# Kernel tuning notes

Hardware: AMD Instinct MI355X
Metric: run time of the kernel (lower is better)

The kernel has to match this reference:

```python
import jax, jax.numpy as jnp
import numpy as np

CHANNEL_ROT = 16
NUM_PIECES = 11
NUM_SQUARES = 64
NUM_FEATURES = NUM_PIECES * NUM_SQUARES * NUM_SQUARES  # 45056
NUM_VECTORS = NUM_SQUARES * NUM_SQUARES               # 4096
VECTOR_DIM = 256
BATCH = 1
TAU = 1.0


def setup_inputs() -> dict:
    key = jax.random.key(0)
    k1, k2, k3 = jax.random.split(key, 3)
    # learned parameter (torch.rand init)
    indices_logits = jax.random.uniform(k1, (NUM_FEATURES, NUM_VECTORS), dtype=jnp.float32)
    # shared vector codebook base (rolled per piece inside reference)
    shared_vectors_base = jax.random.normal(k2, (NUM_VECTORS, VECTOR_DIM), dtype=jnp.float32)
    # explicit gumbel noise so the gumbel-softmax sample is deterministic
    u = jax.random.uniform(k3, (BATCH, NUM_FEATURES, NUM_VECTORS), dtype=jnp.float32,
                           minval=1e-20, maxval=1.0)
    gumbel_noise = -jnp.log(-jnp.log(u))
    # forward arg; only its batch dim is used by the module
    active_features = jnp.zeros((BATCH, NUM_FEATURES), dtype=jnp.int32)
    return {"active_features": active_features,
            "indices_logits": indices_logits,
            "shared_vectors_base": shared_vectors_base,
            "gumbel_noise": gumbel_noise}


def reference(active_features, indices_logits, shared_vectors_base, gumbel_noise):
    B = gumbel_noise.shape[0]
    # per-piece shared vectors: channel-rolled copies of the base codebook (P, V, D)
    sv = jnp.stack([jnp.roll(shared_vectors_base, p * CHANNEL_ROT, axis=1)
                    for p in range(NUM_PIECES)])
    # soft gumbel-softmax sample over the NUM_VECTORS category dim: (B, F, V)
    probs = jax.nn.softmax((indices_logits[None, :, :] + gumbel_noise) / TAU, axis=-1)
    # per-piece einsum 'bqv,vd->bd' == sum probs over q first, then contract v
    q = NUM_FEATURES // NUM_PIECES  # 4096 features per piece
    piece_mass = probs.reshape(B, NUM_PIECES, q, NUM_VECTORS).sum(axis=2)  # (B, P, V)
    position_embedding = jnp.einsum('bpv,pvd->bd', piece_mass, sv)  # (B, D)
    return position_embedding
```

## Files before the change

kernel.cpp:

```cpp
#include <hip/hip_runtime.h>

#define V_DIM   4096
#define D_DIM   256
#define P_CNT   11
#define NB      128
#define ROWS_PB 32
#define P2_BLK  128
#define P2_ROWS 32

__global__ __launch_bounds__(256) void phase1_softmax_mass(
    const float* __restrict__ logits,
    const float* __restrict__ gumbel,
    float* __restrict__ mass)
{
    const int t    = threadIdx.x;
    const int lane = t & 63;
    const int wid  = t >> 6;
    const int b    = blockIdx.x;
    const int p    = b >> 7;
    const int sub  = b & (NB - 1);
    const size_t row0 = (size_t)p * V_DIM + (size_t)sub * ROWS_PB;

    __shared__ float red[8];

    float acc[16];
#pragma unroll
    for (int k = 0; k < 16; ++k) acc[k] = 0.f;

    const float4* lg = (const float4*)(logits + row0 * (size_t)V_DIM);
    const float4* gn = (const float4*)(gumbel + row0 * (size_t)V_DIM);

    float4 a[4], g[4];
#pragma unroll
    for (int k = 0; k < 4; ++k) {
        a[k] = lg[t + 256 * k];
        g[k] = gn[t + 256 * k];
    }

    for (int r = 0; r < ROWS_PB; ++r) {
        float4 a2[4], g2[4];
        const bool more = (r + 1 < ROWS_PB);
        if (more) {
            const float4* lg2 = lg + (size_t)(r + 1) * 1024;
            const float4* gn2 = gn + (size_t)(r + 1) * 1024;
#pragma unroll
            for (int k = 0; k < 4; ++k) {
                a2[k] = lg2[t + 256 * k];
                g2[k] = gn2[t + 256 * k];
            }
        }

        float e[16];
        float s = 0.f;
#pragma unroll
        for (int k = 0; k < 4; ++k) {
            e[4 * k + 0] = __expf(a[k].x + g[k].x);
            e[4 * k + 1] = __expf(a[k].y + g[k].y);
            e[4 * k + 2] = __expf(a[k].z + g[k].z);
            e[4 * k + 3] = __expf(a[k].w + g[k].w);
            s += (e[4 * k + 0] + e[4 * k + 1]) + (e[4 * k + 2] + e[4 * k + 3]);
        }

#pragma unroll
        for (int off = 32; off >= 1; off >>= 1)
            s += __shfl_xor(s, off, 64);
        const int slot = (r & 1) << 2;
        if (lane == 0) red[slot + wid] = s;
        __syncthreads();
        s = (red[slot + 0] + red[slot + 1]) + (red[slot + 2] + red[slot + 3]);
        const float inv = 1.f / s;

#pragma unroll
        for (int k = 0; k < 16; ++k) acc[k] += e[k] * inv;

        if (more) {
#pragma unroll
            for (int k = 0; k < 4; ++k) { a[k] = a2[k]; g[k] = g2[k]; }
        }
    }

    float* mp = mass + (size_t)p * V_DIM;
#pragma unroll
    for (int k = 0; k < 4; ++k) {
        const int j = 4 * (t + 256 * k);
        atomicAdd(mp + j + 0, acc[4 * k + 0]);
        atomicAdd(mp + j + 1, acc[4 * k + 1]);
        atomicAdd(mp + j + 2, acc[4 * k + 2]);
        atomicAdd(mp + j + 3, acc[4 * k + 3]);
    }
}

__global__ __launch_bounds__(256) void phase2_contract(
    const float* __restrict__ mass,
    const float* __restrict__ base,
    float* __restrict__ partial)
{
    __shared__ float sv[P2_ROWS][D_DIM];
    __shared__ float mt[P_CNT][P2_ROWS];

    const int t  = threadIdx.x;
    const int b  = blockIdx.x;
    const int v0 = b * P2_ROWS;

    const float4* bp  = (const float4*)(base + (size_t)v0 * D_DIM);
    float4*       svp = (float4*)&sv[0][0];
#pragma unroll
    for (int k = 0; k < 8; ++k) svp[t + 256 * k] = bp[t + 256 * k];

    for (int i = t; i < P_CNT * P2_ROWS; i += 256) {
        const int p  = i / P2_ROWS;
        const int vv = i - p * P2_ROWS;
        mt[p][vv] = mass[(size_t)p * V_DIM + v0 + vv];
    }
    __syncthreads();

    float a = 0.f;
    for (int v = 0; v < P2_ROWS; ++v) {
#pragma unroll
        for (int p = 0; p < P_CNT; ++p)
            a += mt[p][v] * sv[v][(t - 16 * p) & 255];
    }
    partial[(size_t)b * D_DIM + t] = a;
}

__global__ __launch_bounds__(256) void phase3_reduce(
    const float* __restrict__ partial,
    float* __restrict__ out)
{
    const int t = threadIdx.x;
    float s = 0.f;
#pragma unroll 8
    for (int b = 0; b < P2_BLK; ++b) s += partial[(size_t)b * D_DIM + t];
    out[t] = s;
}

extern "C" void kernel_launch(void* const* d_in, const int* in_sizes, int n_in,
                              void* d_out, int out_size, void* d_ws, size_t ws_size,
                              hipStream_t stream)
{
    const float* logits = (const float*)d_in[1];
    const float* base   = (const float*)d_in[2];
    const float* gumbel = (const float*)d_in[3];
    float* out = (float*)d_out;

    float* mass    = (float*)d_ws;
    float* partial = mass + (size_t)P_CNT * V_DIM;

    hipMemsetAsync(d_ws, 0, (size_t)P_CNT * V_DIM * sizeof(float), stream);

    phase1_softmax_mass<<<dim3(P_CNT * NB), 256, 0, stream>>>(logits, gumbel, mass);
    phase2_contract<<<dim3(P2_BLK), 256, 0, stream>>>(mass, base, partial);
    phase3_reduce<<<dim3(1), 256, 0, stream>>>(partial, out);
}
```

Measured before the change: 287.4 us.

## Replace atomic mass accumulation with per-block partials and a separate reduction kernel

Phase 1 blocks now write their 4096-wide partial mass vectors to a workspace buffer with float4 stores instead of issuing scalar float atomics into a shared per-piece array. A new reduction kernel sums the 128 partials per piece, which also removes the memset. The per-row __syncthreads is swapped for a raw s_waitcnt plus s_barrier. The cost is about 23 MB of extra workspace writes and reads plus one more kernel launch, traded against atomic contention.

```diff
diff --git a/kernel.cpp b/kernel.cpp
--- a/kernel.cpp
+++ b/kernel.cpp
@@ -5,21 +5,20 @@
 #define P_CNT   11
 #define NB      128
 #define ROWS_PB 32
+#define NBLK    (P_CNT * NB)
 #define P2_BLK  128
 #define P2_ROWS 32
 
-__global__ __launch_bounds__(256) void phase1_softmax_mass(
+__global__ __launch_bounds__(256) void phase1_softmax_part(
     const float* __restrict__ logits,
     const float* __restrict__ gumbel,
-    float* __restrict__ mass)
+    float* __restrict__ part)
 {
     const int t    = threadIdx.x;
     const int lane = t & 63;
     const int wid  = t >> 6;
     const int b    = blockIdx.x;
-    const int p    = b >> 7;
-    const int sub  = b & (NB - 1);
-    const size_t row0 = (size_t)p * V_DIM + (size_t)sub * ROWS_PB;
+    const size_t row0 = (size_t)b * ROWS_PB;
 
     __shared__ float red[8];
 
@@ -66,9 +65,12 @@
             s += __shfl_xor(s, off, 64);
         const int slot = (r & 1) << 2;
         if (lane == 0) red[slot + wid] = s;
-        __syncthreads();
+        asm volatile("s_waitcnt lgkmcnt(0)" ::: "memory");
+        __builtin_amdgcn_s_barrier();
+        asm volatile("" ::: "memory");
         s = (red[slot + 0] + red[slot + 1]) + (red[slot + 2] + red[slot + 3]);
         const float inv = 1.f / s;
+
 
 #pragma unroll
         for (int k = 0; k < 16; ++k) acc[k] += e[k] * inv;
@@ -79,15 +81,24 @@
         }
     }
 
-    float* mp = mass + (size_t)p * V_DIM;
+    float4* pp = (float4*)(part + (size_t)b * V_DIM);
 #pragma unroll
-    for (int k = 0; k < 4; ++k) {
-        const int j = 4 * (t + 256 * k);
-        atomicAdd(mp + j + 0, acc[4 * k + 0]);
-        atomicAdd(mp + j + 1, acc[4 * k + 1]);
-        atomicAdd(mp + j + 2, acc[4 * k + 2]);
-        atomicAdd(mp + j + 3, acc[4 * k + 3]);
-    }
+    for (int k = 0; k < 4; ++k)
+        pp[t + 256 * k] = make_float4(acc[4 * k + 0], acc[4 * k + 1],
+                                      acc[4 * k + 2], acc[4 * k + 3]);
+}
+
+__global__ __launch_bounds__(256) void phase1b_reduce_mass(
+    const float* __restrict__ part,
+    float* __restrict__ mass)
+{
+    const int v = blockIdx.x * 256 + threadIdx.x;
+    const int p = blockIdx.y;
+    const float* pp = part + (size_t)p * NB * V_DIM + v;
+    float s = 0.f;
+#pragma unroll 8
+    for (int sub = 0; sub < NB; ++sub) s += pp[(size_t)sub * V_DIM];
+    mass[(size_t)p * V_DIM + v] = s;
 }
 
 __global__ __launch_bounds__(256) void phase2_contract(
@@ -143,12 +154,12 @@
     const float* gumbel = (const float*)d_in[3];
     float* out = (float*)d_out;
 
-    float* mass    = (float*)d_ws;
+    float* part    = (float*)d_ws;
+    float* mass    = part + (size_t)NBLK * V_DIM;
     float* partial = mass + (size_t)P_CNT * V_DIM;
 
-    hipMemsetAsync(d_ws, 0, (size_t)P_CNT * V_DIM * sizeof(float), stream);
-
-    phase1_softmax_mass<<<dim3(P_CNT * NB), 256, 0, stream>>>(logits, gumbel, mass);
+    phase1_softmax_part<<<dim3(NBLK), 256, 0, stream>>>(logits, gumbel, part);
+    phase1b_reduce_mass<<<dim3(V_DIM / 256, P_CNT), 256, 0, stream>>>(part, mass);
     phase2_contract<<<dim3(P2_BLK), 256, 0, stream>>>(mass, base, partial);
     phase3_reduce<<<dim3(1), 256, 0, stream>>>(partial, out);
 }
```

After: 297.1 us. 3.4% more time.
